# Kernel optimization log

Measured on AMD Instinct MI355X. Metric: run time of the kernel, lower is better.

## Reference

```python
import jax, jax.numpy as jnp
import numpy as np

N_ATOMS = 2_000_000
N_STRUCT = 16_384

def _leaky(x):
    return jnp.where(x >= 0, x, 0.01 * x)

def setup_inputs() -> dict:
    key = jax.random.key(0)
    ks = jax.random.split(key, 16)
    atom_prop = jax.random.normal(ks[0], (N_ATOMS, 3), dtype=jnp.float32)
    pos = jax.random.normal(ks[1], (N_ATOMS, 3), dtype=jnp.float32)
    # well-conditioned cells: identity + small perturbation (must be invertible)
    cell = jnp.eye(3, dtype=jnp.float32)[None] + 0.1 * jax.random.normal(ks[2], (N_STRUCT, 3, 3), dtype=jnp.float32)
    batch = jnp.sort(jax.random.randint(ks[3], (N_ATOMS,), 0, N_STRUCT, dtype=jnp.int32))
    s = 0.1
    w0 = s * jax.random.normal(ks[4], (3, 3), dtype=jnp.float32); b0 = jnp.zeros((3,), jnp.float32)
    w1 = jnp.eye(3, dtype=jnp.float32); b1 = jnp.zeros((3,), jnp.float32)
    w1n = jnp.eye(3, dtype=jnp.float32); b1n = jnp.zeros((3,), jnp.float32)
    w2a = s * jax.random.normal(ks[5], (32, 90), dtype=jnp.float32); b2a = jnp.zeros((32,), jnp.float32)
    w2b = s * jax.random.normal(ks[6], (16, 32), dtype=jnp.float32); b2b = jnp.zeros((16,), jnp.float32)
    w2c = s * jax.random.normal(ks[7], (6, 16), dtype=jnp.float32); b2c = jnp.zeros((6,), jnp.float32)
    return dict(atom_prop=atom_prop, pos=pos, cell=cell, batch=batch,
                w0=w0, b0=b0, w1=w1, b1=b1, w1n=w1n, b1n=b1n,
                w2a=w2a, b2a=b2a, w2b=w2b, b2b=b2b, w2c=w2c, b2c=b2c)

def reference(atom_prop, pos, cell, batch, w0, b0, w1, b1, w1n, b1n, w2a, b2a, w2b, b2b, w2c, b2c):
    # cell outer product features: [S,9] -> [S,81], gathered per atom
    cr = cell.reshape(-1, 9)
    cell_ravel = (cr[:, :, None] * cr[:, None, :]).reshape(-1, 81)[batch]  # [N,81]
    cell_inv = jnp.linalg.inv(cell)  # [S,3,3]
    frac_pos = jnp.einsum('nd,nde->ne', pos, cell_inv[batch])  # [N,3]
    threshold = frac_pos - jnp.floor(frac_pos) - 0.5
    atom_prop3 = _leaky(atom_prop @ w0.T + b0)
    t1 = jax.nn.relu(threshold @ w1.T + b1) * atom_prop3
    t2 = jax.nn.relu((-threshold) @ w1n.T + b1n) * atom_prop3
    h = jnp.concatenate((atom_prop, t1, t2, cell_ravel), axis=1)  # [N,90]
    h = jax.nn.relu(h @ w2a.T + b2a)
    h = _leaky(h @ w2b.T + b2b)
    h = h @ w2c.T + b2c  # [N,6]
    stress = jax.ops.segment_sum(h, batch, num_segments=N_STRUCT)  # [S,6]
    return stress
```

## Files before the change

### kernel.cpp

```cpp
#include <hip/hip_runtime.h>
#include <limits.h>

#define BLOCK 256
#define CHUNK 2
#define SPAN  64
#define PERSIST_BLOCKS 2048

typedef float v2f __attribute__((ext_vector_type(2)));

__device__ __forceinline__ v2f pk_fma(v2f a, v2f b, v2f c) {
    return __builtin_elementwise_fma(a, b, c);
}
__device__ __forceinline__ float leaky_(float x){ return x >= 0.f ? x : 0.01f*x; }

#define L_W2AI   0
#define L_W2BT   320
#define L_W2CT   832
#define L_B2B    960
#define L_B2C    976
#define L_W013   984
#define WTAB_SZ  1024
#define L_ACC    1024
#define L_TOT    (1024 + SPAN*6)

__global__ void prep_kernel(const float* __restrict__ cell,
                            const float* __restrict__ w2a,
                            const float* __restrict__ b2a,
                            const float* __restrict__ w2b,
                            const float* __restrict__ w2c,
                            const float* __restrict__ w0, const float* __restrict__ b0,
                            const float* __restrict__ w1, const float* __restrict__ b1,
                            const float* __restrict__ w1n, const float* __restrict__ b1n,
                            const float* __restrict__ b2b, const float* __restrict__ b2c,
                            float* __restrict__ ci_out,
                            float* __restrict__ cc_out,
                            float* __restrict__ wtab,
                            float* __restrict__ out_zero,
                            int S)
{
    __shared__ float sw[2880];
    int tid = threadIdx.x;
    int gid = blockIdx.x * blockDim.x + tid;

    #pragma unroll
    for (int t = 0; t < 3; t++) {
        int idx = tid + t*256;
        if (idx < 720) ((float4*)sw)[idx] = ((const float4*)w2a)[idx];
    }

    if (gid < S * 6) out_zero[gid] = 0.f;

    if (gid < 320) {
        int kp = gid / 20, idx = gid % 20;
        int j = idx >> 1, h = idx & 1;
        wtab[L_W2AI + gid] = (idx < 18) ? w2a[(2*kp + h)*90 + j] : 0.f;
    } else if (gid < 832) {
        int t = gid - 320; int k = t >> 4, m = t & 15;
        wtab[gid] = w2b[m*32 + k];
    } else if (gid < 960) {
        int t = gid - 832; int m = t >> 3, p = t & 7;
        wtab[gid] = (p < 6) ? w2c[p*16 + m] : 0.f;
    } else if (gid < 976) {
        wtab[gid] = b2b[gid - 960];
    } else if (gid < 984) {
        int t = gid - 976; wtab[gid] = (t < 6) ? b2c[t] : 0.f;
    } else if (gid < 1024) {
        int t = gid - 984;
        if (t < 36) {
            int mat = t / 12, rr = t % 12, r = rr >> 2, c = rr & 3;
            const float* W = (mat == 0) ? w0 : (mat == 1) ? w1 : w1n;
            const float* B = (mat == 0) ? b0 : (mat == 1) ? b1 : b1n;
            wtab[gid] = (c < 3) ? W[r*3 + c] : B[r];
        } else wtab[gid] = 0.f;
    }

    __syncthreads();

    int s = gid >> 5;
    if (s >= S) return;
    int k = gid & 31;

    float cr[9];
    #pragma unroll
    for (int j = 0; j < 9; j++) cr[j] = cell[s*9 + j];

    if (k == 0) {
        float a=cr[0],b=cr[1],c=cr[2],d=cr[3],e=cr[4],f=cr[5],g=cr[6],h=cr[7],i=cr[8];
        float A = e*i - f*h;
        float B = f*g - d*i;
        float C = d*h - e*g;
        float det = a*A + b*B + c*C;
        float r = 1.0f / det;
        float* o = ci_out + s*12;
        o[0] = A*r;         o[1] = (c*h - b*i)*r; o[2] = (b*f - c*e)*r;
        o[3] = B*r;         o[4] = (a*i - c*g)*r; o[5] = (c*d - a*f)*r;
        o[6] = C*r;         o[7] = (b*g - a*h)*r; o[8] = (a*e - b*d)*r;
        o[9] = 0.f; o[10] = 0.f; o[11] = 0.f;
    }

    float acc = b2a[k];
    const float* wr = sw + k*90 + 9;
    #pragma unroll
    for (int j1 = 0; j1 < 9; j1++) {
        float c1 = cr[j1];
        #pragma unroll
        for (int j2 = 0; j2 < 9; j2++)
            acc = fmaf(c1 * cr[j2], wr[j1*9 + j2], acc);
    }
    cc_out[s*32 + k] = acc;
}

__global__ __launch_bounds__(BLOCK)
void main_kernel(const float* __restrict__ atom_prop,
                 const float* __restrict__ pos,
                 const int*   __restrict__ batch,
                 const float* __restrict__ ci_ws,
                 const float* __restrict__ cc_ws,
                 const float* __restrict__ wtab,
                 float* __restrict__ out,
                 int N, int S, int ntiles)
{
    __shared__ float lds[L_TOT];
    int tid = threadIdx.x;

    ((float4*)lds)[tid] = ((const float4*)wtab)[tid];

    for (int tile = blockIdx.x; tile < ntiles; tile += gridDim.x) {
        long long blk_base = (long long)tile * (BLOCK * CHUNK);
        int s0 = batch[(blk_base < N) ? blk_base : (N - 1)];

        for (int t = tid; t < SPAN*6; t += BLOCK) lds[L_ACC + t] = 0.f;
        __syncthreads();

        long long base = blk_base + (long long)tid * CHUNK;
        bool any = (base < N);

        int   sv[CHUNK];
        float PX[CHUNK], PY[CHUNK], PZ[CHUNK];
        float AX[CHUNK], AY[CHUNK], AZ[CHUNK];

        if (any && base + CHUNK <= N) {
            int2 bb = *(const int2*)(batch + base);
            sv[0] = bb.x; sv[1] = bb.y;
            const float2* pp = (const float2*)(pos + 3*base);
            float2 p0 = pp[0], p1 = pp[1], p2 = pp[2];
            PX[0]=p0.x; PY[0]=p0.y; PZ[0]=p1.x;
            PX[1]=p1.y; PY[1]=p2.x; PZ[1]=p2.y;
            const float2* ap = (const float2*)(atom_prop + 3*base);
            float2 a0 = ap[0], a1 = ap[1], a2 = ap[2];
            AX[0]=a0.x; AY[0]=a0.y; AZ[0]=a1.x;
            AX[1]=a1.y; AY[1]=a2.x; AZ[1]=a2.y;
        } else {
            #pragma unroll
            for (int t = 0; t < CHUNK; t++) {
                long long i = base + t;
                bool ok = any && (i < N);
                sv[t] = ok ? batch[i] : -1;
                PX[t] = ok ? pos[3*i]   : 0.f;
                PY[t] = ok ? pos[3*i+1] : 0.f;
                PZ[t] = ok ? pos[3*i+2] : 0.f;
                AX[t] = ok ? atom_prop[3*i]   : 0.f;
                AY[t] = ok ? atom_prop[3*i+1] : 0.f;
                AZ[t] = ok ? atom_prop[3*i+2] : 0.f;
            }
        }

        const float* ccp[CHUNK];
        #pragma unroll
        for (int t = 0; t < CHUNK; t++) {
            int s = sv[t] < 0 ? 0 : sv[t];
            ccp[t] = cc_ws + (size_t)s*32;
        }
        float4 c4n[CHUNK];
        #pragma unroll
        for (int t = 0; t < CHUNK; t++) c4n[t] = *(const float4*)(ccp[t]);

        v2f h2[CHUNK][9];
        {
            const float4* q0 = (const float4*)(lds + L_W013);
            const float4* q1 = (const float4*)(lds + L_W013 + 12);
            const float4* q2 = (const float4*)(lds + L_W013 + 24);
            int   cur_s = -1;
            float ci[9];
            #pragma unroll
            for (int t = 0; t < CHUNK; t++) {
                int s = sv[t];
                if (s < 0) {
                    #pragma unroll
                    for (int j = 0; j < 9; j++) h2[t][j] = 0.f;
                    continue;
                }
                if (s != cur_s) {
                    cur_s = s;
                    const float4* cip = (const float4*)(ci_ws + (size_t)s*12);
                    float4 c0 = cip[0], c1 = cip[1], c2 = cip[2];
                    ci[0]=c0.x; ci[1]=c0.y; ci[2]=c0.z; ci[3]=c0.w;
                    ci[4]=c1.x; ci[5]=c1.y; ci[6]=c1.z; ci[7]=c1.w;
                    ci[8]=c2.x;
                }
                float px = PX[t], py = PY[t], pz = PZ[t];
                float ax = AX[t], ay = AY[t], az = AZ[t];

                float f0 = fmaf(px, ci[0], fmaf(py, ci[3], pz*ci[6]));
                float f1 = fmaf(px, ci[1], fmaf(py, ci[4], pz*ci[7]));
                float f2 = fmaf(px, ci[2], fmaf(py, ci[5], pz*ci[8]));
                float t0 = f0 - floorf(f0) - 0.5f;
                float t1 = f1 - floorf(f1) - 0.5f;
                float t2 = f2 - floorf(f2) - 0.5f;

                h2[t][0].x = h2[t][0].y = ax;
                h2[t][1].x = h2[t][1].y = ay;
                h2[t][2].x = h2[t][2].y = az;
                #pragma unroll
                for (int r = 0; r < 3; r++) {
                    float4 a0 = q0[r], a1 = q1[r], a2 = q2[r];
                    float ap3 = leaky_(fmaf(ax, a0.x, fmaf(ay, a0.y, fmaf(az, a0.z, a0.w))));
                    float d1  = fmaf(t0, a1.x, fmaf(t1, a1.y, fmaf(t2, a1.z, a1.w)));
                    float d2  = a2.w - fmaf(t0, a2.x, fmaf(t1, a2.y, t2*a2.z));
                    float v1 = fmaxf(d1, 0.f) * ap3;
                    float v2 = fmaxf(d2, 0.f) * ap3;
                    h2[t][3+r].x = h2[t][3+r].y = v1;
                    h2[t][6+r].x = h2[t][6+r].y = v2;
                }
            }
        }

        v2f vv[CHUNK][8];
        {
            const v2f* b2b2 = (const v2f*)(lds + L_B2B);
            #pragma unroll
            for (int t = 0; t < CHUNK; t++)
                #pragma unroll
                for (int m2 = 0; m2 < 8; m2++) vv[t][m2] = b2b2[m2];
        }

        #pragma unroll
        for (int kb = 0; kb < 8; kb++) {
            float4 c4[CHUNK];
            #pragma unroll
            for (int t = 0; t < CHUNK; t++) c4[t] = c4n[t];
            if (kb < 7) {
                #pragma unroll
                for (int t = 0; t < CHUNK; t++) c4n[t] = *(const float4*)(ccp[t] + (kb+1)*4);
            }

            #pragma unroll
            for (int h = 0; h < 2; h++) {
                int kp = 2*kb + h;
                const v2f* wI  = (const v2f*)(lds + L_W2AI + kp*20);
                const v2f* wb0 = (const v2f*)(lds + L_W2BT + (2*kp)*16);
                const v2f* wb1 = (const v2f*)(lds + L_W2BT + (2*kp+1)*16);
                #pragma unroll
                for (int t = 0; t < CHUNK; t++) {
                    v2f u2;
                    u2.x = h ? c4[t].z : c4[t].x;
                    u2.y = h ? c4[t].w : c4[t].y;
                    #pragma unroll
                    for (int j = 0; j < 9; j++) u2 = pk_fma(h2[t][j], wI[j], u2);
                    v2f zero = 0.f;
                    u2 = __builtin_elementwise_max(u2, zero);
                    v2f ux; ux.x = u2.x; ux.y = u2.x;
                    v2f uy; uy.x = u2.y; uy.y = u2.y;
                    #pragma unroll
                    for (int m2 = 0; m2 < 8; m2++) {
                        vv[t][m2] = pk_fma(ux, wb0[m2], vv[t][m2]);
                        vv[t][m2] = pk_fma(uy, wb1[m2], vv[t][m2]);
                    }
                }
            }
        }

        {
            v2f zero = 0.f, small = 0.01f;
            #pragma unroll
            for (int t = 0; t < CHUNK; t++)
                #pragma unroll
                for (int m2 = 0; m2 < 8; m2++) {
                    v2f mx = __builtin_elementwise_max(vv[t][m2], zero);
                    v2f mn = __builtin_elementwise_min(vv[t][m2], zero);
                    vv[t][m2] = pk_fma(mn, small, mx);
                }
        }

        v2f oo[CHUNK][3];
        {
            const v2f* b2c2 = (const v2f*)(lds + L_B2C);
            #pragma unroll
            for (int t = 0; t < CHUNK; t++)
                #pragma unroll
                for (int p2 = 0; p2 < 3; p2++) oo[t][p2] = b2c2[p2];
        }
        #pragma unroll
        for (int m2 = 0; m2 < 8; m2++) {
            const v2f* wc0 = (const v2f*)(lds + L_W2CT + (2*m2)*8);
            const v2f* wc1 = (const v2f*)(lds + L_W2CT + (2*m2+1)*8);
            #pragma unroll
            for (int t = 0; t < CHUNK; t++) {
                v2f vm = vv[t][m2];
                v2f a; a.x = vm.x; a.y = vm.x;
                v2f b; b.x = vm.y; b.y = vm.y;
                #pragma unroll
                for (int p2 = 0; p2 < 3; p2++)
                    oo[t][p2] = pk_fma(a, wc0[p2], pk_fma(b, wc1[p2], oo[t][p2]));
            }
        }

        const int SENT = INT_MAX;
        int fs;
        float fin[6];
        {
            int sA = sv[0], sB = sv[1];
            if (sA < 0) {
                fs = SENT;
                #pragma unroll
                for (int p = 0; p < 6; p++) fin[p] = 0.f;
            } else if (sB == sA) {
                fs = sA;
                fin[0] = oo[0][0].x + oo[1][0].x; fin[1] = oo[0][0].y + oo[1][0].y;
                fin[2] = oo[0][1].x + oo[1][1].x; fin[3] = oo[0][1].y + oo[1][1].y;
                fin[4] = oo[0][2].x + oo[1][2].x; fin[5] = oo[0][2].y + oo[1][2].y;
            } else {
                float v0[6] = {oo[0][0].x, oo[0][0].y, oo[0][1].x, oo[0][1].y, oo[0][2].x, oo[0][2].y};
                int idx = sA - s0;
                if (idx >= 0 && idx < SPAN) {
                    #pragma unroll
                    for (int p = 0; p < 6; p++) atomicAdd(&lds[L_ACC + idx*6 + p], v0[p]);
                } else {
                    #pragma unroll
                    for (int p = 0; p < 6; p++) atomicAdd(out + (size_t)sA*6 + p, v0[p]);
                }
                if (sB >= 0) {
                    fs = sB;
                    fin[0] = oo[1][0].x; fin[1] = oo[1][0].y;
                    fin[2] = oo[1][1].x; fin[3] = oo[1][1].y;
                    fin[4] = oo[1][2].x; fin[5] = oo[1][2].y;
                } else {
                    fs = SENT;
                    #pragma unroll
                    for (int p = 0; p < 6; p++) fin[p] = 0.f;
                }
            }
        }

        int lane = tid & 63;
        #pragma unroll
        for (int d = 1; d < 64; d <<= 1) {
            int ks = __shfl_up(fs, d);
            bool pred = (lane >= d) && (ks == fs);
            #pragma unroll
            for (int p = 0; p < 6; p++) {
                float vp = __shfl_up(fin[p], d);
                fin[p] += pred ? vp : 0.f;
            }
        }
        {
            int sn = __shfl_down(fs, 1);
            bool tail = (lane == 63) || (sn != fs);
            if (tail && fs != SENT) {
                int idx = fs - s0;
                if (idx >= 0 && idx < SPAN) {
                    #pragma unroll
                    for (int p = 0; p < 6; p++) atomicAdd(&lds[L_ACC + idx*6 + p], fin[p]);
                } else {
                    #pragma unroll
                    for (int p = 0; p < 6; p++) atomicAdd(out + (size_t)fs*6 + p, fin[p]);
                }
            }
        }

        __syncthreads();

        for (int e = tid; e < SPAN*6; e += BLOCK) {
            int idx = e / 6, p = e - idx*6;
            int sg = s0 + idx;
            float v = lds[L_ACC + e];
            if (sg < S && v != 0.f) atomicAdd(out + (size_t)sg*6 + p, v);
        }

        __syncthreads();
    }
}

extern "C" void kernel_launch(void* const* d_in, const int* in_sizes, int n_in,
                              void* d_out, int out_size, void* d_ws, size_t ws_size,
                              hipStream_t stream)
{
    const float* atom_prop = (const float*)d_in[0];
    const float* pos       = (const float*)d_in[1];
    const float* cell      = (const float*)d_in[2];
    const int*   batch     = (const int*)  d_in[3];
    const float* w0  = (const float*)d_in[4];
    const float* b0  = (const float*)d_in[5];
    const float* w1  = (const float*)d_in[6];
    const float* b1  = (const float*)d_in[7];
    const float* w1n = (const float*)d_in[8];
    const float* b1n = (const float*)d_in[9];
    const float* w2a = (const float*)d_in[10];
    const float* b2a = (const float*)d_in[11];
    const float* w2b = (const float*)d_in[12];
    const float* b2b = (const float*)d_in[13];
    const float* w2c = (const float*)d_in[14];
    const float* b2c = (const float*)d_in[15];

    int N = in_sizes[3];
    int S = in_sizes[2] / 9;

    float* out   = (float*)d_out;
    float* ci_ws = (float*)d_ws;
    float* cc_ws = ci_ws + (size_t)S*12;
    float* wtab  = cc_ws + (size_t)S*32;

    int prep_threads = S * 32;
    prep_kernel<<<(prep_threads + 255)/256, 256, 0, stream>>>(
        cell, w2a, b2a, w2b, w2c, w0, b0, w1, b1, w1n, b1n, b2b, b2c,
        ci_ws, cc_ws, wtab, out, S);

    int tile_atoms = BLOCK * CHUNK;
    int ntiles = (N + tile_atoms - 1) / tile_atoms;
    int grid = ntiles < PERSIST_BLOCKS ? ntiles : PERSIST_BLOCKS;
    main_kernel<<<grid, BLOCK, 0, stream>>>(atom_prop, pos, batch,
                                            ci_ws, cc_ws, wtab, out, N, S, ntiles);
}
```

Baseline: 172.9 us.

## Pack two atoms per packed-FMA lane instead of two hidden units

Reorganizes the MLP so each v2f packed FMA operates on the same weight for two atoms (atom-major vectorization) rather than two hidden units of one atom. The weight table is re-laid out (w2a padded to 12 per row, biases duplicated) so weights are loaded as float4 and splatted, and the cc prefetch double-buffering is dropped in favour of direct per-kb loads. This is meant to remove the lane-swizzle broadcasts (ux/uy, a/b) and halve the accumulator arrays, at the cost of more scalar LDS reads and losing the explicit prefetch of cell features.

Result: slower. 178.2 us (+3.1%).

```diff
diff --git a/kernel.cpp b/kernel.cpp
--- a/kernel.cpp
+++ b/kernel.cpp
@@ -11,17 +11,18 @@
 __device__ __forceinline__ v2f pk_fma(v2f a, v2f b, v2f c) {
     return __builtin_elementwise_fma(a, b, c);
 }
+__device__ __forceinline__ v2f sp(float w){ v2f r; r.x = w; r.y = w; return r; }
 __device__ __forceinline__ float leaky_(float x){ return x >= 0.f ? x : 0.01f*x; }
 
-#define L_W2AI   0
-#define L_W2BT   320
-#define L_W2CT   832
-#define L_B2B    960
-#define L_B2C    976
-#define L_W013   984
-#define WTAB_SZ  1024
-#define L_ACC    1024
-#define L_TOT    (1024 + SPAN*6)
+#define L_W2A    0
+#define L_W2BT   384
+#define L_W2CT   896
+#define L_B2B2   1024
+#define L_B2C2   1056
+#define L_W013   1072
+#define WTAB_SZ  1120
+#define L_ACC    1120
+#define L_TOT    (1120 + SPAN*6)
 
 __global__ void prep_kernel(const float* __restrict__ cell,
                             const float* __restrict__ w2a,
@@ -50,22 +51,22 @@
 
     if (gid < S * 6) out_zero[gid] = 0.f;
 
-    if (gid < 320) {
-        int kp = gid / 20, idx = gid % 20;
-        int j = idx >> 1, h = idx & 1;
-        wtab[L_W2AI + gid] = (idx < 18) ? w2a[(2*kp + h)*90 + j] : 0.f;
-    } else if (gid < 832) {
-        int t = gid - 320; int k = t >> 4, m = t & 15;
+    if (gid < 384) {
+        int k = gid / 12, j = gid % 12;
+        wtab[gid] = (j < 9) ? w2a[k*90 + j] : 0.f;
+    } else if (gid < 896) {
+        int t = gid - 384; int k = t >> 4, m = t & 15;
         wtab[gid] = w2b[m*32 + k];
-    } else if (gid < 960) {
-        int t = gid - 832; int m = t >> 3, p = t & 7;
+    } else if (gid < 1024) {
+        int t = gid - 896; int m = t >> 3, p = t & 7;
         wtab[gid] = (p < 6) ? w2c[p*16 + m] : 0.f;
-    } else if (gid < 976) {
-        wtab[gid] = b2b[gid - 960];
-    } else if (gid < 984) {
-        int t = gid - 976; wtab[gid] = (t < 6) ? b2c[t] : 0.f;
-    } else if (gid < 1024) {
-        int t = gid - 984;
+    } else if (gid < 1056) {
+        int t = gid - 1024; wtab[gid] = b2b[t >> 1];
+    } else if (gid < 1072) {
+        int t = gid - 1056; int p = t >> 1;
+        wtab[gid] = (p < 6) ? b2c[p] : 0.f;
+    } else if (gid < 1120) {
+        int t = gid - 1072;
         if (t < 36) {
             int mat = t / 12, rr = t % 12, r = rr >> 2, c = rr & 3;
             const float* W = (mat == 0) ? w0 : (mat == 1) ? w1 : w1n;
@@ -110,6 +111,43 @@
     cc_out[s*32 + k] = acc;
 }
 
+__device__ __forceinline__ void do_k(const float* ldsw, int k, float cA, float cB,
+                                     const v2f* h2, v2f* vv)
+{
+    const float4* wa = (const float4*)(ldsw + L_W2A + k*12);
+    float4 a0 = wa[0], a1 = wa[1], a2 = wa[2];
+    v2f u; u.x = cA; u.y = cB;
+    u = pk_fma(h2[0], sp(a0.x), u);
+    u = pk_fma(h2[1], sp(a0.y), u);
+    u = pk_fma(h2[2], sp(a0.z), u);
+    u = pk_fma(h2[3], sp(a0.w), u);
+    u = pk_fma(h2[4], sp(a1.x), u);
+    u = pk_fma(h2[5], sp(a1.y), u);
+    u = pk_fma(h2[6], sp(a1.z), u);
+    u = pk_fma(h2[7], sp(a1.w), u);
+    u = pk_fma(h2[8], sp(a2.x), u);
+    v2f zero = 0.f;
+    u = __builtin_elementwise_max(u, zero);
+    const float4* wb = (const float4*)(ldsw + L_W2BT + k*16);
+    float4 b0 = wb[0], b1 = wb[1], b2 = wb[2], b3 = wb[3];
+    vv[0]  = pk_fma(u, sp(b0.x), vv[0]);
+    vv[1]  = pk_fma(u, sp(b0.y), vv[1]);
+    vv[2]  = pk_fma(u, sp(b0.z), vv[2]);
+    vv[3]  = pk_fma(u, sp(b0.w), vv[3]);
+    vv[4]  = pk_fma(u, sp(b1.x), vv[4]);
+    vv[5]  = pk_fma(u, sp(b1.y), vv[5]);
+    vv[6]  = pk_fma(u, sp(b1.z), vv[6]);
+    vv[7]  = pk_fma(u, sp(b1.w), vv[7]);
+    vv[8]  = pk_fma(u, sp(b2.x), vv[8]);
+    vv[9]  = pk_fma(u, sp(b2.y), vv[9]);
+    vv[10] = pk_fma(u, sp(b2.z), vv[10]);
+    vv[11] = pk_fma(u, sp(b2.w), vv[11]);
+    vv[12] = pk_fma(u, sp(b3.x), vv[12]);
+    vv[13] = pk_fma(u, sp(b3.y), vv[13]);
+    vv[14] = pk_fma(u, sp(b3.z), vv[14]);
+    vv[15] = pk_fma(u, sp(b3.w), vv[15]);
+}
+
 __global__ __launch_bounds__(BLOCK)
 void main_kernel(const float* __restrict__ atom_prop,
                  const float* __restrict__ pos,
@@ -124,6 +162,7 @@
     int tid = threadIdx.x;
 
     ((float4*)lds)[tid] = ((const float4*)wtab)[tid];
+    if (tid < 24) ((float4*)lds)[256 + tid] = ((const float4*)wtab)[256 + tid];
 
     for (int tile = blockIdx.x; tile < ntiles; tile += gridDim.x) {
         long long blk_base = (long long)tile * (BLOCK * CHUNK);
@@ -165,17 +204,10 @@
             }
         }
 
-        const float* ccp[CHUNK];
-        #pragma unroll
-        for (int t = 0; t < CHUNK; t++) {
-            int s = sv[t] < 0 ? 0 : sv[t];
-            ccp[t] = cc_ws + (size_t)s*32;
-        }
-        float4 c4n[CHUNK];
-        #pragma unroll
-        for (int t = 0; t < CHUNK; t++) c4n[t] = *(const float4*)(ccp[t]);
-
-        v2f h2[CHUNK][9];
+        const float* cc0 = cc_ws + (size_t)(sv[0] < 0 ? 0 : sv[0])*32;
+        const float* cc1 = cc_ws + (size_t)(sv[1] < 0 ? 0 : sv[1])*32;
+
+        float hv[CHUNK][9];
         {
             const float4* q0 = (const float4*)(lds + L_W013);
             const float4* q1 = (const float4*)(lds + L_W013 + 12);
@@ -187,7 +219,7 @@
                 int s = sv[t];
                 if (s < 0) {
                     #pragma unroll
-                    for (int j = 0; j < 9; j++) h2[t][j] = 0.f;
+                    for (int j = 0; j < 9; j++) hv[t][j] = 0.f;
                     continue;
                 }
                 if (s != cur_s) {
@@ -208,101 +240,66 @@
                 float t1 = f1 - floorf(f1) - 0.5f;
                 float t2 = f2 - floorf(f2) - 0.5f;
 
-                h2[t][0].x = h2[t][0].y = ax;
-                h2[t][1].x = h2[t][1].y = ay;
-                h2[t][2].x = h2[t][2].y = az;
+                hv[t][0] = ax; hv[t][1] = ay; hv[t][2] = az;
                 #pragma unroll
                 for (int r = 0; r < 3; r++) {
                     float4 a0 = q0[r], a1 = q1[r], a2 = q2[r];
                     float ap3 = leaky_(fmaf(ax, a0.x, fmaf(ay, a0.y, fmaf(az, a0.z, a0.w))));
                     float d1  = fmaf(t0, a1.x, fmaf(t1, a1.y, fmaf(t2, a1.z, a1.w)));
                     float d2  = a2.w - fmaf(t0, a2.x, fmaf(t1, a2.y, t2*a2.z));
-                    float v1 = fmaxf(d1, 0.f) * ap3;
-                    float v2 = fmaxf(d2, 0.f) * ap3;
-                    h2[t][3+r].x = h2[t][3+r].y = v1;
-                    h2[t][6+r].x = h2[t][6+r].y = v2;
-                }
-            }
-        }
-
-        v2f vv[CHUNK][8];
-        {
-            const v2f* b2b2 = (const v2f*)(lds + L_B2B);
-            #pragma unroll
-            for (int t = 0; t < CHUNK; t++)
-                #pragma unroll
-                for (int m2 = 0; m2 < 8; m2++) vv[t][m2] = b2b2[m2];
+                    hv[t][3+r] = fmaxf(d1, 0.f) * ap3;
+                    hv[t][6+r] = fmaxf(d2, 0.f) * ap3;
+                }
+            }
+        }
+        v2f h2[9];
+        #pragma unroll
+        for (int j = 0; j < 9; j++) { h2[j].x = hv[0][j]; h2[j].y = hv[1][j]; }
+
+        v2f vv[16];
+        {
+            const v2f* bb2 = (const v2f*)(lds + L_B2B2);
+            #pragma unroll
+            for (int m = 0; m < 16; m++) vv[m] = bb2[m];
         }
 
         #pragma unroll
         for (int kb = 0; kb < 8; kb++) {
-            float4 c4[CHUNK];
-            #pragma unroll
-            for (int t = 0; t < CHUNK; t++) c4[t] = c4n[t];
-            if (kb < 7) {
-                #pragma unroll
-                for (int t = 0; t < CHUNK; t++) c4n[t] = *(const float4*)(ccp[t] + (kb+1)*4);
-            }
-
-            #pragma unroll
-            for (int h = 0; h < 2; h++) {
-                int kp = 2*kb + h;
-                const v2f* wI  = (const v2f*)(lds + L_W2AI + kp*20);
-                const v2f* wb0 = (const v2f*)(lds + L_W2BT + (2*kp)*16);
-                const v2f* wb1 = (const v2f*)(lds + L_W2BT + (2*kp+1)*16);
-                #pragma unroll
-                for (int t = 0; t < CHUNK; t++) {
-                    v2f u2;
-                    u2.x = h ? c4[t].z : c4[t].x;
-                    u2.y = h ? c4[t].w : c4[t].y;
-                    #pragma unroll
-                    for (int j = 0; j < 9; j++) u2 = pk_fma(h2[t][j], wI[j], u2);
-                    v2f zero = 0.f;
-                    u2 = __builtin_elementwise_max(u2, zero);
-                    v2f ux; ux.x = u2.x; ux.y = u2.x;
-                    v2f uy; uy.x = u2.y; uy.y = u2.y;
-                    #pragma unroll
-                    for (int m2 = 0; m2 < 8; m2++) {
-                        vv[t][m2] = pk_fma(ux, wb0[m2], vv[t][m2]);
-                        vv[t][m2] = pk_fma(uy, wb1[m2], vv[t][m2]);
-                    }
-                }
-            }
+            float4 ca = *(const float4*)(cc0 + kb*4);
+            float4 cb = *(const float4*)(cc1 + kb*4);
+            do_k(lds, kb*4 + 0, ca.x, cb.x, h2, vv);
+            do_k(lds, kb*4 + 1, ca.y, cb.y, h2, vv);
+            do_k(lds, kb*4 + 2, ca.z, cb.z, h2, vv);
+            do_k(lds, kb*4 + 3, ca.w, cb.w, h2, vv);
         }
 
         {
             v2f zero = 0.f, small = 0.01f;
             #pragma unroll
-            for (int t = 0; t < CHUNK; t++)
-                #pragma unroll
-                for (int m2 = 0; m2 < 8; m2++) {
-                    v2f mx = __builtin_elementwise_max(vv[t][m2], zero);
-                    v2f mn = __builtin_elementwise_min(vv[t][m2], zero);
-                    vv[t][m2] = pk_fma(mn, small, mx);
-                }
-        }
-
-        v2f oo[CHUNK][3];
-        {
-            const v2f* b2c2 = (const v2f*)(lds + L_B2C);
-            #pragma unroll
-            for (int t = 0; t < CHUNK; t++)
-                #pragma unroll
-                for (int p2 = 0; p2 < 3; p2++) oo[t][p2] = b2c2[p2];
+            for (int m = 0; m < 16; m++) {
+                v2f mx = __builtin_elementwise_max(vv[m], zero);
+                v2f mn = __builtin_elementwise_min(vv[m], zero);
+                vv[m] = pk_fma(mn, small, mx);
+            }
+        }
+
+        v2f oo[6];
+        {
+            const v2f* bc2 = (const v2f*)(lds + L_B2C2);
+            #pragma unroll
+            for (int p = 0; p < 6; p++) oo[p] = bc2[p];
         }
         #pragma unroll
-        for (int m2 = 0; m2 < 8; m2++) {
-            const v2f* wc0 = (const v2f*)(lds + L_W2CT + (2*m2)*8);
-            const v2f* wc1 = (const v2f*)(lds + L_W2CT + (2*m2+1)*8);
-            #pragma unroll
-            for (int t = 0; t < CHUNK; t++) {
-                v2f vm = vv[t][m2];
-                v2f a; a.x = vm.x; a.y = vm.x;
-                v2f b; b.x = vm.y; b.y = vm.y;
-                #pragma unroll
-                for (int p2 = 0; p2 < 3; p2++)
-                    oo[t][p2] = pk_fma(a, wc0[p2], pk_fma(b, wc1[p2], oo[t][p2]));
-            }
+        for (int m = 0; m < 16; m++) {
+            const float4* wc = (const float4*)(lds + L_W2CT + m*8);
+            float4 c0 = wc[0], c1 = wc[1];
+            v2f vm = vv[m];
+            oo[0] = pk_fma(vm, sp(c0.x), oo[0]);
+            oo[1] = pk_fma(vm, sp(c0.y), oo[1]);
+            oo[2] = pk_fma(vm, sp(c0.z), oo[2]);
+            oo[3] = pk_fma(vm, sp(c0.w), oo[3]);
+            oo[4] = pk_fma(vm, sp(c1.x), oo[4]);
+            oo[5] = pk_fma(vm, sp(c1.y), oo[5]);
         }
 
         const int SENT = INT_MAX;
@@ -316,24 +313,21 @@
                 for (int p = 0; p < 6; p++) fin[p] = 0.f;
             } else if (sB == sA) {
                 fs = sA;
-                fin[0] = oo[0][0].x + oo[1][0].x; fin[1] = oo[0][0].y + oo[1][0].y;
-                fin[2] = oo[0][1].x + oo[1][1].x; fin[3] = oo[0][1].y + oo[1][1].y;
-                fin[4] = oo[0][2].x + oo[1][2].x; fin[5] = oo[0][2].y + oo[1][2].y;
+                #pragma unroll
+                for (int p = 0; p < 6; p++) fin[p] = oo[p].x + oo[p].y;
             } else {
-                float v0[6] = {oo[0][0].x, oo[0][0].y, oo[0][1].x, oo[0][1].y, oo[0][2].x, oo[0][2].y};
                 int idx = sA - s0;
                 if (idx >= 0 && idx < SPAN) {
                     #pragma unroll
-                    for (int p = 0; p < 6; p++) atomicAdd(&lds[L_ACC + idx*6 + p], v0[p]);
+                    for (int p = 0; p < 6; p++) atomicAdd(&lds[L_ACC + idx*6 + p], oo[p].x);
                 } else {
                     #pragma unroll
-                    for (int p = 0; p < 6; p++) atomicAdd(out + (size_t)sA*6 + p, v0[p]);
+                    for (int p = 0; p < 6; p++) atomicAdd(out + (size_t)sA*6 + p, oo[p].x);
                 }
                 if (sB >= 0) {
                     fs = sB;
-                    fin[0] = oo[1][0].x; fin[1] = oo[1][0].y;
-                    fin[2] = oo[1][1].x; fin[3] = oo[1][1].y;
-                    fin[4] = oo[1][2].x; fin[5] = oo[1][2].y;
+                    #pragma unroll
+                    for (int p = 0; p < 6; p++) fin[p] = oo[p].y;
                 } else {
                     fs = SENT;
                     #pragma unroll
```
